# Optimization experiments

Measured on AMD Instinct MI355X. Metric: run time of the kernel, lower is better.

## Reference

```python
import jax, jax.numpy as jnp
import numpy as np

# S4 (liquid-S4, degree=1) forward: diagonal bilinear-discretized SSM kernel,
# FFT global convolution, D skip, liquid correction term, gelu + output linear.

LIQUID_DEGREE = 1


def _forward(u, log_dt, w_re, w_im, B_re, B_im, C_re, C_im, D, W, bias):
    Bb, H, L = u.shape
    dt = jnp.exp(log_dt)                              # (H,)
    w = w_re + 1j * w_im                              # (H, N/2)
    w = jnp.concatenate([w, jnp.conj(w)], axis=-1)    # _conj -> (H, N)
    Bp = B_re + 1j * B_im
    Bp = jnp.concatenate([Bp, jnp.conj(Bp)], axis=-1)  # (H, N)
    Cp = C_re + 1j * C_im
    Cp = jnp.concatenate([Cp, jnp.conj(Cp)], axis=-1)  # (C, H, N)

    denom = 1.0 - 0.5 * dt[:, None] * w               # (H, N)
    dA = (1.0 + 0.5 * dt[:, None] * w) / denom        # bilinear discretization
    dB = dt[:, None] * Bp / denom                     # (H, N), matches diag_embed formula

    # SSM convolution kernel k[c,h,l] = Re( sum_n C[c,h,n] * dB[h,n] * dA[h,n]^l )
    ell = jnp.arange(L)
    V = jnp.exp(jnp.log(dA)[:, :, None] * ell)        # (H, N, L) Vandermonde
    k = jnp.einsum('chn,hn,hnl->chl', Cp, dB, V).real.astype(u.dtype)  # (C, H, L)

    # FFT circular-to-linear convolution (pad to 2L)
    n = 2 * L
    k_f = jnp.fft.rfft(k, n=n)                        # (C, H, L+1)
    u_f = jnp.fft.rfft(u, n=n)                        # (B, H, L+1)
    y = jnp.fft.irfft(u_f[:, None] * k_f[None], n=n)[..., :L]  # (B, C, H, L)
    y = y + u[:, None] * D[None, :, :, None]          # D skip: 'bhl,ch->bchl'

    # Liquid correction terms
    us = u
    dBl = dB
    for _ in range(LIQUID_DEGREE):
        us = us * jnp.pad(us[..., :-1], ((0, 0), (0, 0), (1, 0)))   # u_t * u_{t-1}
        dBl = dBl * jnp.sum(dBl, axis=-1, keepdims=True)            # (dB1*dB2).sum(2)
        dCB = jnp.einsum('chn,hn->ch', Cp, dBl).real                # (C, H) real part (.float())
        y = y + us[:, None] * dCB[None, :, :, None]                 # (B, C, H, L)

    y = y.reshape(Bb, -1, L)                          # (B, C*H, L)
    y = jax.nn.gelu(y)
    y = jnp.einsum('oh,bhl->bol', W, y) + bias[None, :, None]  # output_linear (1x1 conv)
    return y


def setup_inputs() -> dict:
    key = jax.random.key(0)
    ks = jax.random.split(key, 8)
    Bsz, H, L, N2, C = 4, 256, 4096, 32, 1
    u = jax.random.normal(ks[0], (Bsz, H, L), jnp.float32)
    # dt log-uniform in [1e-3, 1e-1] (standard S4 init)
    lo, hi = np.log(1e-3), np.log(1e-1)
    log_dt = (lo + (hi - lo) * jax.random.uniform(ks[1], (H,))).astype(jnp.float32)
    # S4D-Lin style eigenvalues: w = -1/2 + i*pi*n (stable: Re(w) < 0)
    w_re = -0.5 * jnp.ones((H, N2), jnp.float32)
    w_im = jnp.tile(jnp.pi * jnp.arange(N2, dtype=jnp.float32), (H, 1))
    B_re = jax.random.normal(ks[2], (H, N2), jnp.float32)
    B_im = jax.random.normal(ks[3], (H, N2), jnp.float32)
    C_re = jax.random.normal(ks[4], (C, H, N2), jnp.float32) * 0.5
    C_im = jax.random.normal(ks[5], (C, H, N2), jnp.float32) * 0.5
    D = jax.random.normal(ks[6], (C, H), jnp.float32)
    W = jax.random.normal(ks[7], (H, C * H), jnp.float32) / np.sqrt(C * H)
    bias = jnp.zeros((H,), jnp.float32)
    return {"u": u, "log_dt": log_dt, "w_re": w_re, "w_im": w_im,
            "B_re": B_re, "B_im": B_im, "C_re": C_re, "C_im": C_im,
            "D": D, "W": W, "bias": bias}


def reference(u, log_dt, w_re, w_im, B_re, B_im, C_re, C_im, D, W, bias):
    return _forward(u, log_dt, w_re, w_im, B_re, B_im, C_re, C_im, D, W, bias)
```

## Files before the change

### kernel.cpp

```cpp
#include <hip/hip_runtime.h>
#include <math.h>


#define H 256
#define LSEQ 4096
#define NB 4
#define NMODES 32
#define T 64
#define NC 64
#define NSEG 4
#define SEGC 16

typedef _Float16 f16;
typedef _Float16 f16x2 __attribute__((ext_vector_type(2)));
typedef _Float16 f16x8 __attribute__((ext_vector_type(8)));
typedef float f32x4 __attribute__((ext_vector_type(4)));
union U16x8 { f16x8 v; f16x2 h[4]; uint4 q; };

static __device__ __forceinline__ f16x2 pk(float a, float b) {
    typedef __fp16 fp16x2n __attribute__((ext_vector_type(2)));
    fp16x2n r = __builtin_amdgcn_cvt_pkrtz(a, b);
    return __builtin_bit_cast(f16x2, r);
}

__global__ __launch_bounds__(512) void k_setup(
    const float* __restrict__ log_dt, const float* __restrict__ w_re, const float* __restrict__ w_im,
    const float* __restrict__ B_re, const float* __restrict__ B_im,
    const float* __restrict__ C_re, const float* __restrict__ C_im,
    const float* __restrict__ W,
    float2* __restrict__ P, f16* __restrict__ Mh, f16* __restrict__ Wh,
    float2* __restrict__ dAT, float* __restrict__ dCB)
{
    __shared__ float ks_lds[T];
    __shared__ float ERe_lds[NMODES * T];
    __shared__ float EIm_lds[NMODES * T];

    int tid = threadIdx.x;
    int h = blockIdx.x;
    int n = tid & 31;
    int pg = tid >> 5;
    int hn = h * NMODES + n;

    if (tid < 256) Wh[h * 256 + tid] = (f16)W[h * 256 + tid];

    double dt = exp((double)log_dt[h]);
    double zr = 0.5 * dt * (double)w_re[hn], zi = 0.5 * dt * (double)w_im[hn];
    double dr = 1.0 - zr, di = -zi;
    double dn = dr * dr + di * di;
    double nr = 1.0 + zr, ni = zi;
    double dAr = (nr * dr + ni * di) / dn, dAi = (ni * dr - nr * di) / dn;
    double tbr = dt * (double)B_re[hn], tbi = dt * (double)B_im[hn];
    double dBr = (tbr * dr + tbi * di) / dn, dBi = (tbi * dr - tbr * di) / dn;
    double Cr = (double)C_re[hn], Ci = (double)C_im[hn];
    double CBr = Cr * dBr - Ci * dBi, CBi = Cr * dBi + Ci * dBr;

    double d2r = dAr*dAr - dAi*dAi,  d2i = 2.0*dAr*dAi;
    double d4r = d2r*d2r - d2i*d2i,  d4i = 2.0*d2r*d2i;
    double d8r = d4r*d4r - d4i*d4i,  d8i = 2.0*d4r*d4i;
    double d16r= d8r*d8r - d8i*d8i,  d16i= 2.0*d8r*d8i;
    double d32r= d16r*d16r - d16i*d16i, d32i = 2.0*d16r*d16i;
    double ar = 1.0, ai = 0.0;
    if (pg & 1) { double t0 = ar*d4r - ai*d4i;  ai = ar*d4i + ai*d4r;  ar = t0; }
    if (pg & 2) { double t0 = ar*d8r - ai*d8i;  ai = ar*d8i + ai*d8r;  ar = t0; }
    if (pg & 4) { double t0 = ar*d16r - ai*d16i; ai = ar*d16i + ai*d16r; ar = t0; }
    if (pg & 8) { double t0 = ar*d32r - ai*d32i; ai = ar*d32i + ai*d32r; ar = t0; }

    #pragma unroll
    for (int i = 0; i < 4; ++i) {
        int p = pg * 4 + i;
        double pr = dBr * ar - dBi * ai, pi = dBr * ai + dBi * ar;
        P[(h * T + p) * NMODES + n] = make_float2((float)pr, (float)pi);
        float q = (float)(CBr * ar - CBi * ai);
        #pragma unroll
        for (int m = 16; m >= 1; m >>= 1) q += __shfl_xor(q, m);
        if (n == 0) ks_lds[p] = 2.0f * q;
        double nar = ar * dAr - ai * dAi;
        ai = ar * dAi + ai * dAr; ar = nar;
        ERe_lds[n * T + p] = (float)(2.0 * (Cr * ar - Ci * ai));
        EIm_lds[n * T + p] = (float)(2.0 * (Cr * ai + Ci * ar));
    }
    if (pg == 15) dAT[hn] = make_float2((float)ar, (float)ai);
    if (pg == 0) {
        float s1 = (float)dBr, s2 = (float)CBr;
        #pragma unroll
        for (int m = 16; m >= 1; m >>= 1) { s1 += __shfl_xor(s1, m); s2 += __shfl_xor(s2, m); }
        if (n == 0) dCB[h] = 4.0f * s1 * s2;
    }
    __syncthreads();

    int t = tid >> 3, kq = tid & 7;
    U16x8 w4[2];
    #pragma unroll
    for (int i = 0; i < 16; ++i) {
        int k = kq * 16 + i;
        float val;
        if (k < 64)       val = (k <= t) ? ks_lds[t - k] : 0.f;
        else if (k < 96)  val = ERe_lds[(k - 64) * T + t];
        else              val = EIm_lds[(k - 96) * T + t];
        w4[i >> 3].h[(i >> 1) & 3][i & 1] = (f16)val;
    }
    uint4* dst = (uint4*)(Mh + ((size_t)(h * T) + t) * 128 + kq * 16);
    dst[0] = w4[0].q;
    dst[1] = w4[1].q;
}

__global__ __launch_bounds__(256) void k_local(
    const float* __restrict__ u, const float2* __restrict__ P,
    float* __restrict__ SLre, float* __restrict__ SLim)
{
    __shared__ float u_s[64 * 68];
    int tid = threadIdx.x;
    int bh = blockIdx.x;
    int h = bh & (H - 1);

    const float4* uv4 = (const float4*)(u + (size_t)bh * LSEQ);
    #pragma unroll
    for (int it = 0; it < 4; ++it) {
        int f = tid + it * 256;
        int c = f >> 4, j4 = (f & 15) * 4;
        *(float4*)(&u_s[c * 68 + j4]) = uv4[f];
    }
    __syncthreads();

    int n16 = tid & 15, cq = tid >> 4;
    float2 acc[4][2];
    #pragma unroll
    for (int i = 0; i < 4; ++i) { acc[i][0] = make_float2(0.f,0.f); acc[i][1] = make_float2(0.f,0.f); }

    const float4* P4 = (const float4*)P;
    size_t prow = (size_t)h * T;
    #pragma unroll 4
    for (int j = 0; j < T; ++j) {
        float4 pv = P4[(prow + (T - 1 - j)) * 16 + n16];
        #pragma unroll
        for (int i = 0; i < 4; ++i) {
            float uval = u_s[(cq * 4 + i) * 68 + j];
            acc[i][0].x += pv.x * uval; acc[i][0].y += pv.y * uval;
            acc[i][1].x += pv.z * uval; acc[i][1].y += pv.w * uval;
        }
    }
    #pragma unroll
    for (int i = 0; i < 4; ++i) {
        int c = cq * 4 + i;
        size_t idx = ((size_t)bh * NC + c) * NMODES + 2 * n16;
        *(float2*)(SLre + idx) = make_float2(acc[i][0].x, acc[i][1].x);
        *(float2*)(SLim + idx) = make_float2(acc[i][0].y, acc[i][1].y);
    }
}

__global__ __launch_bounds__(256) void k_scanA(
    const float2* __restrict__ dAT, float* __restrict__ SLre, float* __restrict__ SLim,
    float2* __restrict__ Carry)
{
    int gid = blockIdx.x * 256 + threadIdx.x;
    int n = gid & 31;
    int seg = (gid >> 5) & 3;
    int bh = gid >> 7;
    int h = bh & (H - 1);
    float2 A = dAT[h * NMODES + n];
    float Sr = 0.f, Si = 0.f;
    size_t base = ((size_t)bh * NC + seg * SEGC) * NMODES + n;
    for (int r = 0; r < SEGC; ++r) {
        size_t idx = base + (size_t)r * NMODES;
        float lr = SLre[idx], li = SLim[idx];
        SLre[idx] = Sr; SLim[idx] = Si;
        float ns = Sr * A.x - Si * A.y + lr;
        Si = Sr * A.y + Si * A.x + li;
        Sr = ns;
    }
    Carry[((size_t)bh * NSEG + seg) * NMODES + n] = make_float2(Sr, Si);
}

__global__ __launch_bounds__(256) void k_scanB(
    const float2* __restrict__ dAT, float* __restrict__ SLre, float* __restrict__ SLim,
    const float2* __restrict__ Carry)
{
    int gid = blockIdx.x * 256 + threadIdx.x;
    int n = gid & 31;
    int seg = (gid >> 5) & 3;
    int bh = gid >> 7;
    int h = bh & (H - 1);
    float2 A = dAT[h * NMODES + n];
    float ar = A.x, ai = A.y;
    #pragma unroll
    for (int s = 0; s < 4; ++s) { float t = ar*ar - ai*ai; ai = 2.f*ar*ai; ar = t; }
    float Er = 0.f, Ei = 0.f;
    const float2* Cb = Carry + (size_t)bh * NSEG * NMODES + n;
    for (int j = 0; j < seg; ++j) {
        float2 C = Cb[(size_t)j * NMODES];
        float t = Er * ar - Ei * ai + C.x;
        Ei = Er * ai + Ei * ar + C.y;
        Er = t;
    }
    float Vr = Er, Vi = Ei;
    size_t base = ((size_t)bh * NC + seg * SEGC) * NMODES + n;
    for (int r = 0; r < SEGC; ++r) {
        size_t idx = base + (size_t)r * NMODES;
        float lr = SLre[idx], li = SLim[idx];
        SLre[idx] = Vr + lr;
        SLim[idx] = -(Vi + li);
        float t = Vr * A.x - Vi * A.y;
        Vi = Vr * A.y + Vi * A.x;
        Vr = t;
    }
}

__global__ __launch_bounds__(256) void k_main(
    const float* __restrict__ u, const f16* __restrict__ Mh,
    const float* __restrict__ SLre, const float* __restrict__ SLim,
    const float* __restrict__ dCB, const float* __restrict__ D,
    float* __restrict__ YG)
{
    int h = blockIdx.x;
    int tid = threadIdx.x;
    int w = tid >> 6, lane = tid & 63;
    int l15 = lane & 15, g = lane >> 4;

    f32x4 acc[4][4];
    #pragma unroll
    for (int i = 0; i < 4; ++i)
        #pragma unroll
        for (int j = 0; j < 4; ++j) acc[i][j] = (f32x4)0.f;

    const f16* Mbase = Mh + (size_t)h * T * 128;

    #pragma unroll
    for (int s = 0; s < 4; ++s) {
        f16x8 a4[4];
        #pragma unroll
        for (int tt = 0; tt < 4; ++tt)
            a4[tt] = *(const f16x8*)(Mbase + (tt * 16 + l15) * 128 + 32 * s + 8 * g);

        #pragma unroll
        for (int qt = 0; qt < 4; ++qt) {
            int q = w * 64 + qt * 16 + l15;
            int b = q >> 6, c = q & 63;
            U16x8 bf;
            f32x4 lo, hi;
            if (s < 2) {
                int j0 = 32 * s + 8 * g;
                const float* up = u + ((size_t)(b * H + h)) * LSEQ + c * T + j0;
                lo = *(const f32x4*)up;
                hi = *(const f32x4*)(up + 4);
            } else {
                int n0 = 8 * g;
                const float* sp = (s == 2 ? SLre : SLim) +
                                  ((size_t)(b * H + h) * NC + c) * NMODES + n0;
                lo = *(const f32x4*)sp;
                hi = *(const f32x4*)(sp + 4);
            }
            bf.h[0] = pk(lo.x, lo.y);
            bf.h[1] = pk(lo.z, lo.w);
            bf.h[2] = pk(hi.x, hi.y);
            bf.h[3] = pk(hi.z, hi.w);
            #pragma unroll
            for (int tt = 0; tt < 4; ++tt)
                acc[tt][qt] = __builtin_amdgcn_mfma_f32_16x16x32_f16(a4[tt], bf.v, acc[tt][qt], 0, 0, 0);
        }
    }

    float Dh = D[h], dCBh = dCB[h];
    #pragma unroll
    for (int tt = 0; tt < 4; ++tt) {
        #pragma unroll
        for (int qt = 0; qt < 4; ++qt) {
            int q = w * 64 + qt * 16 + l15;
            int b = q >> 6, c = q & 63;
            int l0 = c * T + tt * 16 + g * 4;
            const float* ub = u + ((size_t)(b * H + h)) * LSEQ;
            f32x4 uv = *(const f32x4*)(ub + l0);
            float up0 = (l0 == 0) ? 0.f : ub[l0 - 1];
            float ups[4] = {up0, uv.x, uv.y, uv.z};
            f32x4 out4;
            #pragma unroll
            for (int r = 0; r < 4; ++r) {
                float y = acc[tt][qt][r] + Dh * uv[r] + dCBh * uv[r] * ups[r];
                float y3 = y * y * y;
                out4[r] = 0.5f * y * (1.f + tanhf(0.7978845608028654f * (y + 0.044715f * y3)));
            }
            *(f32x4*)(YG + ((size_t)(b * H + h)) * LSEQ + l0) = out4;
        }
    }
}

__global__ __launch_bounds__(256) void k_out(
    const float* __restrict__ YG, const f16* __restrict__ Wh,
    const float* __restrict__ bias, float* __restrict__ out)
{
    int tid = threadIdx.x;
    int w = tid >> 6, lane = tid & 63;
    int l15 = lane & 15, g = lane >> 4;
    int o0 = blockIdx.y * 32 + (w >> 1) * 16;
    int Lbase = blockIdx.x * 256 + (w & 1) * 128;

    f16x8 a8[8];
    #pragma unroll
    for (int s = 0; s < 8; ++s)
        a8[s] = *(const f16x8*)(Wh + (size_t)(o0 + l15) * 256 + 32 * s + 8 * g);

    f32x4 acc[8];
    #pragma unroll
    for (int i = 0; i < 8; ++i) acc[i] = (f32x4)0.f;

    #pragma unroll
    for (int s = 0; s < 8; ++s) {
        int h0 = 32 * s + 8 * g;
        #pragma unroll
        for (int lt = 0; lt < 8; ++lt) {
            int L = Lbase + lt * 16 + l15;
            int b = L >> 12, l = L & 4095;
            const float* yp = YG + (size_t)b * (H * LSEQ) + (size_t)h0 * LSEQ + l;
            float v0 = yp[0];
            float v1 = yp[LSEQ];
            float v2 = yp[2 * LSEQ];
            float v3 = yp[3 * LSEQ];
            float v4 = yp[4 * LSEQ];
            float v5 = yp[5 * LSEQ];
            float v6 = yp[6 * LSEQ];
            float v7 = yp[7 * LSEQ];
            U16x8 bf;
            bf.h[0] = pk(v0, v1);
            bf.h[1] = pk(v2, v3);
            bf.h[2] = pk(v4, v5);
            bf.h[3] = pk(v6, v7);
            acc[lt] = __builtin_amdgcn_mfma_f32_16x16x32_f16(a8[s], bf.v, acc[lt], 0, 0, 0);
        }
    }

    #pragma unroll
    for (int lt = 0; lt < 8; ++lt) {
        int L = Lbase + lt * 16 + l15;
        int b = L >> 12, l = L & 4095;
        #pragma unroll
        for (int r = 0; r < 4; ++r) {
            int o = o0 + g * 4 + r;
            out[((size_t)(b * 256 + o)) * LSEQ + l] = acc[lt][r] + bias[o];
        }
    }
}

extern "C" void kernel_launch(void* const* d_in, const int* in_sizes, int n_in,
                              void* d_out, int out_size, void* d_ws, size_t ws_size,
                              hipStream_t stream) {
    const float* u      = (const float*)d_in[0];
    const float* log_dt = (const float*)d_in[1];
    const float* w_re   = (const float*)d_in[2];
    const float* w_im   = (const float*)d_in[3];
    const float* B_re   = (const float*)d_in[4];
    const float* B_im   = (const float*)d_in[5];
    const float* C_re   = (const float*)d_in[6];
    const float* C_im   = (const float*)d_in[7];
    const float* Dp     = (const float*)d_in[8];
    const float* Wp     = (const float*)d_in[9];
    const float* bias   = (const float*)d_in[10];
    float* out = (float*)d_out;
    float* ws = (float*)d_ws;

    float2* P    = (float2*)(ws);
    f16*    Mh   = (f16*)(ws + 1048576);
    f16*    Wh   = (f16*)(ws + 2097152);
    float2* dAT  = (float2*)(ws + 2129920);
    float*  dCB  = ws + 2146304;
    float*  SLre = ws + 2146560;
    float*  SLim = ws + 4243712;
    float*  YG   = ws + 6340864;
    float2* Carry = (float2*)(ws);

    k_setup<<<H, 512, 0, stream>>>(log_dt, w_re, w_im, B_re, B_im, C_re, C_im,
                                   Wp, P, Mh, Wh, dAT, dCB);
    k_local<<<NB * H, 256, 0, stream>>>(u, P, SLre, SLim);
    k_scanA<<<NB * H * NSEG * NMODES / 256, 256, 0, stream>>>(dAT, SLre, SLim, Carry);
    k_scanB<<<NB * H * NSEG * NMODES / 256, 256, 0, stream>>>(dAT, SLre, SLim, Carry);
    k_main<<<H, 256, 0, stream>>>(u, Mh, SLre, SLim, dCB, Dp, YG);
    dim3 g5(LSEQ * NB / 256, H / 32);
    k_out<<<g5, 256, 0, stream>>>(YG, Wh, bias, out);
}
```

Before: 149.8 us.

## Store gelu output as fp16 and restage output GEMM through LDS

k_main now writes the gelu intermediate as fp16 instead of fp32, which halves the bytes written and later re-read. k_out is restructured so each block covers 32 sequence positions and all 256 output channels. It loads the fp16 activations with vector loads, transposes them through padded LDS and prefetches the next chunk, replacing the strided per-element global gathers. The cost is extra rounding of the intermediate to fp16, which was already converted to fp16 before the MFMA, so accuracy is mostly unchanged. The new layout also re-reads W from global memory in every block.

```diff
diff --git a/kernel.cpp b/kernel.cpp
--- a/kernel.cpp
+++ b/kernel.cpp
@@ -13,9 +13,11 @@
 
 typedef _Float16 f16;
 typedef _Float16 f16x2 __attribute__((ext_vector_type(2)));
+typedef _Float16 f16x4 __attribute__((ext_vector_type(4)));
 typedef _Float16 f16x8 __attribute__((ext_vector_type(8)));
 typedef float f32x4 __attribute__((ext_vector_type(4)));
 union U16x8 { f16x8 v; f16x2 h[4]; uint4 q; };
+union U16x4 { f16x4 v; f16x2 h[2]; };
 
 static __device__ __forceinline__ f16x2 pk(float a, float b) {
     typedef __fp16 fp16x2n __attribute__((ext_vector_type(2)));
@@ -209,7 +211,7 @@
     const float* __restrict__ u, const f16* __restrict__ Mh,
     const float* __restrict__ SLre, const float* __restrict__ SLim,
     const float* __restrict__ dCB, const float* __restrict__ D,
-    float* __restrict__ YG)
+    f16* __restrict__ YG)
 {
     int h = blockIdx.x;
     int tid = threadIdx.x;
@@ -278,63 +280,65 @@
                 float y3 = y * y * y;
                 out4[r] = 0.5f * y * (1.f + tanhf(0.7978845608028654f * (y + 0.044715f * y3)));
             }
-            *(f32x4*)(YG + ((size_t)(b * H + h)) * LSEQ + l0) = out4;
-        }
-    }
-}
-
+            U16x4 o16;
+            o16.h[0] = pk(out4[0], out4[1]);
+            o16.h[1] = pk(out4[2], out4[3]);
+            *(f16x4*)(YG + ((size_t)(b * H + h)) * LSEQ + l0) = o16.v;
+        }
+    }
+}
+
+#define KO_STRIDE 40
 __global__ __launch_bounds__(256) void k_out(
-    const float* __restrict__ YG, const f16* __restrict__ Wh,
+    const f16* __restrict__ YG, const f16* __restrict__ Wh,
     const float* __restrict__ bias, float* __restrict__ out)
 {
+    __shared__ f16 lds_b[32 * KO_STRIDE];
     int tid = threadIdx.x;
     int w = tid >> 6, lane = tid & 63;
     int l15 = lane & 15, g = lane >> 4;
-    int o0 = blockIdx.y * 32 + (w >> 1) * 16;
-    int Lbase = blockIdx.x * 256 + (w & 1) * 128;
-
-    f16x8 a8[8];
-    #pragma unroll
-    for (int s = 0; s < 8; ++s)
-        a8[s] = *(const f16x8*)(Wh + (size_t)(o0 + l15) * 256 + 32 * s + 8 * g);
-
-    f32x4 acc[8];
-    #pragma unroll
-    for (int i = 0; i < 8; ++i) acc[i] = (f32x4)0.f;
-
-    #pragma unroll
-    for (int s = 0; s < 8; ++s) {
-        int h0 = 32 * s + 8 * g;
-        #pragma unroll
-        for (int lt = 0; lt < 8; ++lt) {
-            int L = Lbase + lt * 16 + l15;
-            int b = L >> 12, l = L & 4095;
-            const float* yp = YG + (size_t)b * (H * LSEQ) + (size_t)h0 * LSEQ + l;
-            float v0 = yp[0];
-            float v1 = yp[LSEQ];
-            float v2 = yp[2 * LSEQ];
-            float v3 = yp[3 * LSEQ];
-            float v4 = yp[4 * LSEQ];
-            float v5 = yp[5 * LSEQ];
-            float v6 = yp[6 * LSEQ];
-            float v7 = yp[7 * LSEQ];
-            U16x8 bf;
-            bf.h[0] = pk(v0, v1);
-            bf.h[1] = pk(v2, v3);
-            bf.h[2] = pk(v4, v5);
-            bf.h[3] = pk(v6, v7);
-            acc[lt] = __builtin_amdgcn_mfma_f32_16x16x32_f16(a8[s], bf.v, acc[lt], 0, 0, 0);
-        }
-    }
-
-    #pragma unroll
-    for (int lt = 0; lt < 8; ++lt) {
-        int L = Lbase + lt * 16 + l15;
-        int b = L >> 12, l = L & 4095;
-        #pragma unroll
-        for (int r = 0; r < 4; ++r) {
-            int o = o0 + g * 4 + r;
-            out[((size_t)(b * 256 + o)) * LSEQ + l] = acc[lt][r] + bias[o];
+    int Lb = blockIdx.x * 32;
+    int b = Lb >> 12, lbase = Lb & 4095;
+    int o0 = w * 64;
+
+    int hh = tid >> 3, l4 = (tid & 7) * 4;
+
+    f32x4 acc[4][2];
+    #pragma unroll
+    for (int i = 0; i < 4; ++i) { acc[i][0] = (f32x4)0.f; acc[i][1] = (f32x4)0.f; }
+
+    const f16* ygb = YG + ((size_t)(b * H + hh)) * LSEQ + lbase + l4;
+    f16x4 v = *(const f16x4*)ygb;
+
+    for (int k = 0; k < 8; ++k) {
+        if (k) __syncthreads();
+        #pragma unroll
+        for (int i = 0; i < 4; ++i) lds_b[(l4 + i) * KO_STRIDE + hh] = v[i];
+        if (k < 7) v = *(const f16x4*)(ygb + (size_t)(k + 1) * 32 * LSEQ);
+        __syncthreads();
+
+        f16x8 bf[2];
+        #pragma unroll
+        for (int lt = 0; lt < 2; ++lt)
+            bf[lt] = *(const f16x8*)(&lds_b[(lt * 16 + l15) * KO_STRIDE + 8 * g]);
+        #pragma unroll
+        for (int ot = 0; ot < 4; ++ot) {
+            f16x8 a = *(const f16x8*)(Wh + (size_t)(o0 + ot * 16 + l15) * 256 + k * 32 + 8 * g);
+            acc[ot][0] = __builtin_amdgcn_mfma_f32_16x16x32_f16(a, bf[0], acc[ot][0], 0, 0, 0);
+            acc[ot][1] = __builtin_amdgcn_mfma_f32_16x16x32_f16(a, bf[1], acc[ot][1], 0, 0, 0);
+        }
+    }
+
+    #pragma unroll
+    for (int ot = 0; ot < 4; ++ot) {
+        #pragma unroll
+        for (int lt = 0; lt < 2; ++lt) {
+            int l = lbase + lt * 16 + l15;
+            #pragma unroll
+            for (int r = 0; r < 4; ++r) {
+                int o = o0 + ot * 16 + g * 4 + r;
+                out[((size_t)(b * 256 + o)) * LSEQ + l] = acc[ot][lt][r] + bias[o];
+            }
         }
     }
 }
@@ -363,7 +367,7 @@
     float*  dCB  = ws + 2146304;
     float*  SLre = ws + 2146560;
     float*  SLim = ws + 4243712;
-    float*  YG   = ws + 6340864;
+    f16*    YG16 = (f16*)(ws + 6340864);
     float2* Carry = (float2*)(ws);
 
     k_setup<<<H, 512, 0, stream>>>(log_dt, w_re, w_im, B_re, B_im, C_re, C_im,
@@ -371,7 +375,6 @@
     k_local<<<NB * H, 256, 0, stream>>>(u, P, SLre, SLim);
     k_scanA<<<NB * H * NSEG * NMODES / 256, 256, 0, stream>>>(dAT, SLre, SLim, Carry);
     k_scanB<<<NB * H * NSEG * NMODES / 256, 256, 0, stream>>>(dAT, SLre, SLim, Carry);
-    k_main<<<H, 256, 0, stream>>>(u, Mh, SLre, SLim, dCB, Dp, YG);
-    dim3 g5(LSEQ * NB / 256, H / 32);
-    k_out<<<g5, 256, 0, stream>>>(YG, Wh, bias, out);
-}
+    k_main<<<H, 256, 0, stream>>>(u, Mh, SLre, SLim, dCB, Dp, YG16);
+    k_out<<<NB * LSEQ / 32, 256, 0, stream>>>(YG16, Wh, bias, out);
+}
```

After: 146.9 us. 1.02x faster.
